# Kernel optimization log

Hardware: AMD Instinct MI355X
Metric: run time of the kernel (lower is better)

Reference implementation:

```python
import jax, jax.numpy as jnp
import numpy as np

K_CODES, D_DIM = 512, 64


def setup_inputs() -> dict:
    key = jax.random.key(0)
    k1, k2 = jax.random.split(key)
    x = jax.random.normal(k1, (32, D_DIM, 64, 64), dtype=jnp.float32)  # NCHW
    weight = jax.random.uniform(k2, (K_CODES, D_DIM), minval=-1.0 / K_CODES,
                                maxval=1.0 / K_CODES, dtype=jnp.float32)
    return {"x": x, "weight": weight}


def reference(x, weight):
    K = weight.shape[0]
    xp = jnp.transpose(x, (0, 2, 3, 1))          # [B, H, W, D]
    flat = xp.reshape(-1, weight.shape[1])       # [N, D]
    dist = (jnp.sum(flat * flat, axis=1, keepdims=True)
            + jnp.sum(weight * weight, axis=1)
            - 2.0 * flat @ weight.T)
    idx = jnp.argmin(dist, axis=1)               # [N]
    enc = jax.nn.one_hot(idx, K, dtype=jnp.float32)   # [N, K] one-hot scatter
    quantized = (enc @ weight).reshape(xp.shape)      # matmul codebook lookup
    commit_loss = jnp.mean(jnp.square(jax.lax.stop_gradient(quantized) - xp))
    vq_loss = jnp.mean(jnp.square(quantized - jax.lax.stop_gradient(xp)))
    loss = vq_loss + 1.0 * commit_loss           # commitment_cost = 1.0
    quant_st = xp + jax.lax.stop_gradient(quantized - xp)  # straight-through
    return (loss, jnp.transpose(quant_st, (0, 3, 1, 2)), enc, idx)
```

## Files before the change

kernel.cpp:

```cpp
#include <hip/hip_runtime.h>
#include <cfloat>

#define KC 512
#define DD 64
#define HW 4096
#define NPIX 131072
#define QSIZE 8388608
#define PXB 128
#define NBLK (NPIX / PXB)
#define NTH 512
#define MARGIN 4.0e-3f

typedef short short8 __attribute__((ext_vector_type(8)));
typedef float f32x4 __attribute__((ext_vector_type(4)));
typedef float nfloat4 __attribute__((ext_vector_type(4)));
typedef unsigned long long u64;

__device__ __forceinline__ unsigned short bf16_rne(float f) {
    unsigned int u = __float_as_uint(f);
    u += 0x7FFFu + ((u >> 16) & 1u);
    return (unsigned short)(u >> 16);
}

__global__ __launch_bounds__(NTH, 4) void vq_fused(
    const float* __restrict__ x, const float* __restrict__ w,
    float* __restrict__ out_q, float* __restrict__ out_enc,
    float* __restrict__ out_idx, double* __restrict__ partial) {

  __shared__ uint4 wlds[4096];
  __shared__ float w2s[KC];
  __shared__ u64 candm[PXB][8];
  __shared__ float Xs[PXB];
  __shared__ int sidx[PXB];
  __shared__ float sredf[8];

  const int tid = threadIdx.x;
  const int lane = tid & 63;
  const int wv = tid >> 6;
  const int bix = blockIdx.x;
  const int b = bix >> 5;
  const int p0 = (bix & 31) * PXB;
  const float* xt = x + (size_t)b * (DD * HW) + p0;

  {
    const int k = tid;
    const float* wk = w + k * DD;
    float r0 = __fmul_rn(wk[0], wk[0]), r1 = __fmul_rn(wk[1], wk[1]),
          r2 = __fmul_rn(wk[2], wk[2]), r3 = __fmul_rn(wk[3], wk[3]),
          r4 = __fmul_rn(wk[4], wk[4]), r5 = __fmul_rn(wk[5], wk[5]),
          r6 = __fmul_rn(wk[6], wk[6]), r7 = __fmul_rn(wk[7], wk[7]);
    #pragma unroll
    for (int i = 8; i < DD; i += 8) {
      r0 = __fadd_rn(r0, __fmul_rn(wk[i+0], wk[i+0]));
      r1 = __fadd_rn(r1, __fmul_rn(wk[i+1], wk[i+1]));
      r2 = __fadd_rn(r2, __fmul_rn(wk[i+2], wk[i+2]));
      r3 = __fadd_rn(r3, __fmul_rn(wk[i+3], wk[i+3]));
      r4 = __fadd_rn(r4, __fmul_rn(wk[i+4], wk[i+4]));
      r5 = __fadd_rn(r5, __fmul_rn(wk[i+5], wk[i+5]));
      r6 = __fadd_rn(r6, __fmul_rn(wk[i+6], wk[i+6]));
      r7 = __fadd_rn(r7, __fmul_rn(wk[i+7], wk[i+7]));
    }
    w2s[k] = __fadd_rn(__fadd_rn(__fadd_rn(r0, r1), __fadd_rn(r2, r3)),
                       __fadd_rn(__fadd_rn(r4, r5), __fadd_rn(r6, r7)));
  }

  for (int s = tid; s < 4096; s += NTH) {
    int ct = s >> 7, kc = (s >> 6) & 1, ln = s & 63;
    int n = ln & 15, q = ln >> 4;
    const float* wp = w + (ct * 16 + n) * DD + kc * 32 + q * 8;
    nfloat4 f0 = *(const nfloat4*)(wp);
    nfloat4 f1 = *(const nfloat4*)(wp + 4);
    uint4 u;
    u.x = (unsigned)bf16_rne(f0[0]) | ((unsigned)bf16_rne(f0[1]) << 16);
    u.y = (unsigned)bf16_rne(f0[2]) | ((unsigned)bf16_rne(f0[3]) << 16);
    u.z = (unsigned)bf16_rne(f1[0]) | ((unsigned)bf16_rne(f1[1]) << 16);
    u.w = (unsigned)bf16_rne(f1[2]) | ((unsigned)bf16_rne(f1[3]) << 16);
    wlds[s] = u;
  }
  for (int i = tid; i < PXB * 8; i += NTH) ((u64*)candm)[i] = 0;

  if (tid < PXB) {
    const float* xp = xt + tid;
    float r0 = __fmul_rn(xp[0*HW], xp[0*HW]), r1 = __fmul_rn(xp[1*HW], xp[1*HW]),
          r2 = __fmul_rn(xp[2*HW], xp[2*HW]), r3 = __fmul_rn(xp[3*HW], xp[3*HW]),
          r4 = __fmul_rn(xp[4*HW], xp[4*HW]), r5 = __fmul_rn(xp[5*HW], xp[5*HW]),
          r6 = __fmul_rn(xp[6*HW], xp[6*HW]), r7 = __fmul_rn(xp[7*HW], xp[7*HW]);
    #pragma unroll
    for (int i = 8; i < DD; i += 8) {
      r0 = __fadd_rn(r0, __fmul_rn(xp[(size_t)(i+0)*HW], xp[(size_t)(i+0)*HW]));
      r1 = __fadd_rn(r1, __fmul_rn(xp[(size_t)(i+1)*HW], xp[(size_t)(i+1)*HW]));
      r2 = __fadd_rn(r2, __fmul_rn(xp[(size_t)(i+2)*HW], xp[(size_t)(i+2)*HW]));
      r3 = __fadd_rn(r3, __fmul_rn(xp[(size_t)(i+3)*HW], xp[(size_t)(i+3)*HW]));
      r4 = __fadd_rn(r4, __fmul_rn(xp[(size_t)(i+4)*HW], xp[(size_t)(i+4)*HW]));
      r5 = __fadd_rn(r5, __fmul_rn(xp[(size_t)(i+5)*HW], xp[(size_t)(i+5)*HW]));
      r6 = __fadd_rn(r6, __fmul_rn(xp[(size_t)(i+6)*HW], xp[(size_t)(i+6)*HW]));
      r7 = __fadd_rn(r7, __fmul_rn(xp[(size_t)(i+7)*HW], xp[(size_t)(i+7)*HW]));
    }
    Xs[tid] = __fadd_rn(__fadd_rn(__fadd_rn(r0, r1), __fadd_rn(r2, r3)),
                        __fadd_rn(__fadd_rn(r4, r5), __fadd_rn(r6, r7)));
  }

  const int am = lane & 15, aq = lane >> 4;
  const float* xa = xt + wv * 16 + am;
  short8 a0, a1;
  #pragma unroll
  for (int j = 0; j < 8; ++j) {
    a0[j] = (short)bf16_rne(-2.0f * xa[(size_t)(aq * 8 + j) * HW]);
    a1[j] = (short)bf16_rne(-2.0f * xa[(size_t)(32 + aq * 8 + j) * HW]);
  }

  __syncthreads();

  const short8* wl8 = (const short8*)wlds;
  const int cn = lane & 15;

  float m0 = FLT_MAX, m1 = FLT_MAX, m2 = FLT_MAX, m3 = FLT_MAX;
  for (int ct = 0; ct < 32; ++ct) {
    float wk2 = w2s[ct * 16 + cn];
    f32x4 acc = {wk2, wk2, wk2, wk2};
    acc = __builtin_amdgcn_mfma_f32_16x16x32_bf16(a0, wl8[ct * 128 + lane], acc, 0, 0, 0);
    acc = __builtin_amdgcn_mfma_f32_16x16x32_bf16(a1, wl8[ct * 128 + 64 + lane], acc, 0, 0, 0);
    m0 = fminf(m0, acc[0]); m1 = fminf(m1, acc[1]);
    m2 = fminf(m2, acc[2]); m3 = fminf(m3, acc[3]);
  }
  #pragma unroll
  for (int s = 1; s < 16; s <<= 1) {
    m0 = fminf(m0, __shfl_xor(m0, s));
    m1 = fminf(m1, __shfl_xor(m1, s));
    m2 = fminf(m2, __shfl_xor(m2, s));
    m3 = fminf(m3, __shfl_xor(m3, s));
  }
  const float t0 = m0 + MARGIN, t1 = m1 + MARGIN,
              t2 = m2 + MARGIN, t3 = m3 + MARGIN;

  for (int ct = 0; ct < 32; ++ct) {
    float wk2 = w2s[ct * 16 + cn];
    f32x4 acc = {wk2, wk2, wk2, wk2};
    acc = __builtin_amdgcn_mfma_f32_16x16x32_bf16(a0, wl8[ct * 128 + lane], acc, 0, 0, 0);
    acc = __builtin_amdgcn_mfma_f32_16x16x32_bf16(a1, wl8[ct * 128 + 64 + lane], acc, 0, 0, 0);
    u64 bm0 = __ballot(acc[0] <= t0);
    u64 bm1 = __ballot(acc[1] <= t1);
    u64 bm2 = __ballot(acc[2] <= t2);
    u64 bm3 = __ballot(acc[3] <= t3);
    if (lane < 4) {
      u64 mk = (lane == 0) ? bm0 : (lane == 1) ? bm1 : (lane == 2) ? bm2 : bm3;
      int word = ct >> 2, sh = (ct & 3) * 16;
      #pragma unroll
      for (int q = 0; q < 4; ++q) {
        u64 bits = (mk >> (q * 16)) & 0xFFFFull;
        if (bits) candm[wv * 16 + q * 4 + lane][word] |= bits << sh;
      }
    }
  }
  __syncthreads();

  {
    const int px = tid >> 2, part = tid & 3;
    const float X = Xs[px];
    const float* xr = xt + px;
    float bestd = FLT_MAX; int bk = 1 << 30;
    for (int wd = part * 2; wd < part * 2 + 2; ++wd) {
      u64 msk = candm[px][wd];
      while (msk) {
        int bit = __ffsll((unsigned long long)msk) - 1;
        msk &= msk - 1;
        int k = wd * 64 + bit;
        const float* wp = w + k * DD;
        float P = 0.f;
        #pragma unroll
        for (int dc = 0; dc < 16; ++dc) {
          nfloat4 w4 = *(const nfloat4*)(wp + dc * 4);
          P = __fmaf_rn(xr[(size_t)(dc * 4 + 0) * HW], w4[0], P);
          P = __fmaf_rn(xr[(size_t)(dc * 4 + 1) * HW], w4[1], P);
          P = __fmaf_rn(xr[(size_t)(dc * 4 + 2) * HW], w4[2], P);
          P = __fmaf_rn(xr[(size_t)(dc * 4 + 3) * HW], w4[3], P);
        }
        float dist = __fsub_rn(__fadd_rn(X, w2s[k]), __fadd_rn(P, P));
        if (dist < bestd || (dist == bestd && k < bk)) { bestd = dist; bk = k; }
      }
    }
    float od = __shfl_down(bestd, 1); int ok = __shfl_down(bk, 1);
    if ((lane & 3) < 3 && (od < bestd || (od == bestd && ok < bk))) { bestd = od; bk = ok; }
    od = __shfl_down(bestd, 2); ok = __shfl_down(bk, 2);
    if ((lane & 3) < 2 && (od < bestd || (od == bestd && ok < bk))) { bestd = od; bk = ok; }
    if (part == 0) {
      sidx[px] = bk;
      out_idx[bix * PXB + px] = (float)bk;
    }
  }
  __syncthreads();

  float lsum = 0.f;
  float* qb = out_q + (size_t)b * (DD * HW) + p0;
  for (int i = tid; i < PXB * DD; i += NTH) {
    int d = i >> 7, pp = i & 127;
    float qv = w[sidx[pp] * DD + d];
    float dv = qv - xt[(size_t)d * HW + pp];
    lsum = __fmaf_rn(dv, dv, lsum);
    __builtin_nontemporal_store(qv, qb + (size_t)d * HW + pp);
  }
  #pragma unroll
  for (int off = 32; off > 0; off >>= 1) lsum += __shfl_down(lsum, off);
  if (lane == 0) sredf[wv] = lsum;
  __syncthreads();
  if (tid == 0) {
    double t = 0.0;
    #pragma unroll
    for (int i = 0; i < 8; ++i) t += (double)sredf[i];
    partial[bix] = t;
  }

  float* basep = out_enc + (size_t)bix * (PXB * KC);
  for (int t = tid; t < 16383; t += NTH) {
    int u = 3 + 4 * t;
    nfloat4 v;
    #pragma unroll
    for (int j = 0; j < 4; ++j) {
      int e = u + j;
      v[j] = (sidx[e >> 9] == (e & 511)) ? 1.0f : 0.0f;
    }
    __builtin_nontemporal_store(v, (nfloat4*)(basep + u));
  }
  if (tid < 3) basep[tid] = (sidx[0] == tid) ? 1.0f : 0.0f;
  else if (tid == 3) basep[PXB * KC - 1] = (sidx[127] == 511) ? 1.0f : 0.0f;
}

__global__ void finish_kernel(const double* __restrict__ partial,
                              float* __restrict__ out) {
  int t = threadIdx.x;
  double s = partial[t] + partial[t + 256] + partial[t + 512] + partial[t + 768];
  #pragma unroll
  for (int off = 32; off > 0; off >>= 1) s += __shfl_down(s, off);
  __shared__ double sr[4];
  if ((t & 63) == 0) sr[t >> 6] = s;
  __syncthreads();
  if (t == 0)
    out[0] = (float)(2.0 * (sr[0] + sr[1] + sr[2] + sr[3]) / (double)QSIZE);
}

extern "C" void kernel_launch(void* const* d_in, const int* in_sizes, int n_in,
                              void* d_out, int out_size, void* d_ws, size_t ws_size,
                              hipStream_t stream) {
  const float* x = (const float*)d_in[0];
  const float* w = (const float*)d_in[1];
  float* out = (float*)d_out;
  float* out_q = out + 1;
  float* out_enc = out_q + QSIZE;
  float* out_idx = out_enc + (size_t)NPIX * KC;

  double* partial = (double*)d_ws;

  vq_fused<<<NBLK, NTH, 0, stream>>>(x, w, out_q, out_enc, out_idx, partial);
  finish_kernel<<<1, 256, 0, stream>>>(partial, out);
}
```

Baseline: 391.3 us.

## Hoist codebook prep to a separate kernel and shrink blocks to raise occupancy

Codebook bf16 swizzling and squared-norm computation move out of the per-block prologue into a small prep kernel that writes to workspace. The main kernel drops its 64KB LDS copy of the codebook and reads MFMA B operands directly from global/L2, with 64-pixel blocks of 256 threads and a higher waves-per-EU hint. This removes redundant per-block conversion work and the LDS limit on occupancy. In exchange, every MFMA operand load now goes through the cache hierarchy instead of LDS, and there is an extra kernel launch.

```diff
diff --git a/kernel.cpp b/kernel.cpp
--- a/kernel.cpp
+++ b/kernel.cpp
@@ -6,9 +6,9 @@
 #define HW 4096
 #define NPIX 131072
 #define QSIZE 8388608
-#define PXB 128
+#define PXB 64
 #define NBLK (NPIX / PXB)
-#define NTH 512
+#define NTH 256
 #define MARGIN 4.0e-3f
 
 typedef short short8 __attribute__((ext_vector_type(8)));
@@ -22,29 +22,25 @@
     return (unsigned short)(u >> 16);
 }
 
-__global__ __launch_bounds__(NTH, 4) void vq_fused(
-    const float* __restrict__ x, const float* __restrict__ w,
-    float* __restrict__ out_q, float* __restrict__ out_enc,
-    float* __restrict__ out_idx, double* __restrict__ partial) {
-
-  __shared__ uint4 wlds[4096];
-  __shared__ float w2s[KC];
-  __shared__ u64 candm[PXB][8];
-  __shared__ float Xs[PXB];
-  __shared__ int sidx[PXB];
-  __shared__ float sredf[8];
-
-  const int tid = threadIdx.x;
-  const int lane = tid & 63;
-  const int wv = tid >> 6;
-  const int bix = blockIdx.x;
-  const int b = bix >> 5;
-  const int p0 = (bix & 31) * PXB;
-  const float* xt = x + (size_t)b * (DD * HW) + p0;
-
+__global__ __launch_bounds__(1024) void prep(
+    const float* __restrict__ w, float* __restrict__ w2g,
+    uint4* __restrict__ wswz) {
+  const int gt = blockIdx.x * 1024 + threadIdx.x;
   {
-    const int k = tid;
-    const float* wk = w + k * DD;
+    int ct = gt >> 7, kc = (gt >> 6) & 1, ln = gt & 63;
+    int n = ln & 15, q = ln >> 4;
+    const float* wp = w + (ct * 16 + n) * DD + kc * 32 + q * 8;
+    nfloat4 f0 = *(const nfloat4*)(wp);
+    nfloat4 f1 = *(const nfloat4*)(wp + 4);
+    uint4 u;
+    u.x = (unsigned)bf16_rne(f0[0]) | ((unsigned)bf16_rne(f0[1]) << 16);
+    u.y = (unsigned)bf16_rne(f0[2]) | ((unsigned)bf16_rne(f0[3]) << 16);
+    u.z = (unsigned)bf16_rne(f1[0]) | ((unsigned)bf16_rne(f1[1]) << 16);
+    u.w = (unsigned)bf16_rne(f1[2]) | ((unsigned)bf16_rne(f1[3]) << 16);
+    wswz[gt] = u;
+  }
+  if (gt < KC) {
+    const float* wk = w + gt * DD;
     float r0 = __fmul_rn(wk[0], wk[0]), r1 = __fmul_rn(wk[1], wk[1]),
           r2 = __fmul_rn(wk[2], wk[2]), r3 = __fmul_rn(wk[3], wk[3]),
           r4 = __fmul_rn(wk[4], wk[4]), r5 = __fmul_rn(wk[5], wk[5]),
@@ -60,24 +56,33 @@
       r6 = __fadd_rn(r6, __fmul_rn(wk[i+6], wk[i+6]));
       r7 = __fadd_rn(r7, __fmul_rn(wk[i+7], wk[i+7]));
     }
-    w2s[k] = __fadd_rn(__fadd_rn(__fadd_rn(r0, r1), __fadd_rn(r2, r3)),
-                       __fadd_rn(__fadd_rn(r4, r5), __fadd_rn(r6, r7)));
-  }
-
-  for (int s = tid; s < 4096; s += NTH) {
-    int ct = s >> 7, kc = (s >> 6) & 1, ln = s & 63;
-    int n = ln & 15, q = ln >> 4;
-    const float* wp = w + (ct * 16 + n) * DD + kc * 32 + q * 8;
-    nfloat4 f0 = *(const nfloat4*)(wp);
-    nfloat4 f1 = *(const nfloat4*)(wp + 4);
-    uint4 u;
-    u.x = (unsigned)bf16_rne(f0[0]) | ((unsigned)bf16_rne(f0[1]) << 16);
-    u.y = (unsigned)bf16_rne(f0[2]) | ((unsigned)bf16_rne(f0[3]) << 16);
-    u.z = (unsigned)bf16_rne(f1[0]) | ((unsigned)bf16_rne(f1[1]) << 16);
-    u.w = (unsigned)bf16_rne(f1[2]) | ((unsigned)bf16_rne(f1[3]) << 16);
-    wlds[s] = u;
-  }
+    w2g[gt] = __fadd_rn(__fadd_rn(__fadd_rn(r0, r1), __fadd_rn(r2, r3)),
+                        __fadd_rn(__fadd_rn(r4, r5), __fadd_rn(r6, r7)));
+  }
+}
+
+__global__ __launch_bounds__(NTH, 6) void vq_fused(
+    const float* __restrict__ x, const float* __restrict__ w,
+    const float* __restrict__ w2g, const uint4* __restrict__ wswz,
+    float* __restrict__ out_q, float* __restrict__ out_enc,
+    float* __restrict__ out_idx, double* __restrict__ partial) {
+
+  __shared__ u64 candm[PXB][8];
+  __shared__ float w2l[KC];
+  __shared__ float Xs[PXB];
+  __shared__ int sidx[PXB];
+  __shared__ float sredf[4];
+
+  const int tid = threadIdx.x;
+  const int lane = tid & 63;
+  const int wv = tid >> 6;
+  const int bix = blockIdx.x;
+  const int b = bix >> 6;
+  const int p0 = (bix & 63) * PXB;
+  const float* xt = x + (size_t)b * (DD * HW) + p0;
+
   for (int i = tid; i < PXB * 8; i += NTH) ((u64*)candm)[i] = 0;
+  w2l[tid] = w2g[tid]; w2l[tid + 256] = w2g[tid + 256];
 
   if (tid < PXB) {
     const float* xp = xt + tid;
@@ -111,15 +116,15 @@
 
   __syncthreads();
 
-  const short8* wl8 = (const short8*)wlds;
+  const short8* gw8 = (const short8*)wswz;
   const int cn = lane & 15;
 
   float m0 = FLT_MAX, m1 = FLT_MAX, m2 = FLT_MAX, m3 = FLT_MAX;
   for (int ct = 0; ct < 32; ++ct) {
-    float wk2 = w2s[ct * 16 + cn];
+    float wk2 = w2l[ct * 16 + cn];
     f32x4 acc = {wk2, wk2, wk2, wk2};
-    acc = __builtin_amdgcn_mfma_f32_16x16x32_bf16(a0, wl8[ct * 128 + lane], acc, 0, 0, 0);
-    acc = __builtin_amdgcn_mfma_f32_16x16x32_bf16(a1, wl8[ct * 128 + 64 + lane], acc, 0, 0, 0);
+    acc = __builtin_amdgcn_mfma_f32_16x16x32_bf16(a0, gw8[ct * 128 + lane], acc, 0, 0, 0);
+    acc = __builtin_amdgcn_mfma_f32_16x16x32_bf16(a1, gw8[ct * 128 + 64 + lane], acc, 0, 0, 0);
     m0 = fminf(m0, acc[0]); m1 = fminf(m1, acc[1]);
     m2 = fminf(m2, acc[2]); m3 = fminf(m3, acc[3]);
   }
@@ -134,10 +139,10 @@
               t2 = m2 + MARGIN, t3 = m3 + MARGIN;
 
   for (int ct = 0; ct < 32; ++ct) {
-    float wk2 = w2s[ct * 16 + cn];
+    float wk2 = w2l[ct * 16 + cn];
     f32x4 acc = {wk2, wk2, wk2, wk2};
-    acc = __builtin_amdgcn_mfma_f32_16x16x32_bf16(a0, wl8[ct * 128 + lane], acc, 0, 0, 0);
-    acc = __builtin_amdgcn_mfma_f32_16x16x32_bf16(a1, wl8[ct * 128 + 64 + lane], acc, 0, 0, 0);
+    acc = __builtin_amdgcn_mfma_f32_16x16x32_bf16(a0, gw8[ct * 128 + lane], acc, 0, 0, 0);
+    acc = __builtin_amdgcn_mfma_f32_16x16x32_bf16(a1, gw8[ct * 128 + 64 + lane], acc, 0, 0, 0);
     u64 bm0 = __ballot(acc[0] <= t0);
     u64 bm1 = __ballot(acc[1] <= t1);
     u64 bm2 = __ballot(acc[2] <= t2);
@@ -175,7 +180,7 @@
           P = __fmaf_rn(xr[(size_t)(dc * 4 + 2) * HW], w4[2], P);
           P = __fmaf_rn(xr[(size_t)(dc * 4 + 3) * HW], w4[3], P);
         }
-        float dist = __fsub_rn(__fadd_rn(X, w2s[k]), __fadd_rn(P, P));
+        float dist = __fsub_rn(__fadd_rn(X, w2l[k]), __fadd_rn(P, P));
         if (dist < bestd || (dist == bestd && k < bk)) { bestd = dist; bk = k; }
       }
     }
@@ -193,7 +198,7 @@
   float lsum = 0.f;
   float* qb = out_q + (size_t)b * (DD * HW) + p0;
   for (int i = tid; i < PXB * DD; i += NTH) {
-    int d = i >> 7, pp = i & 127;
+    int d = i >> 6, pp = i & 63;
     float qv = w[sidx[pp] * DD + d];
     float dv = qv - xt[(size_t)d * HW + pp];
     lsum = __fmaf_rn(dv, dv, lsum);
@@ -203,15 +208,12 @@
   for (int off = 32; off > 0; off >>= 1) lsum += __shfl_down(lsum, off);
   if (lane == 0) sredf[wv] = lsum;
   __syncthreads();
-  if (tid == 0) {
-    double t = 0.0;
-    #pragma unroll
-    for (int i = 0; i < 8; ++i) t += (double)sredf[i];
-    partial[bix] = t;
-  }
+  if (tid == 0)
+    partial[bix] = (double)sredf[0] + (double)sredf[1]
+                 + (double)sredf[2] + (double)sredf[3];
 
   float* basep = out_enc + (size_t)bix * (PXB * KC);
-  for (int t = tid; t < 16383; t += NTH) {
+  for (int t = tid; t < 8191; t += NTH) {
     int u = 3 + 4 * t;
     nfloat4 v;
     #pragma unroll
@@ -222,13 +224,15 @@
     __builtin_nontemporal_store(v, (nfloat4*)(basep + u));
   }
   if (tid < 3) basep[tid] = (sidx[0] == tid) ? 1.0f : 0.0f;
-  else if (tid == 3) basep[PXB * KC - 1] = (sidx[127] == 511) ? 1.0f : 0.0f;
+  else if (tid == 3) basep[PXB * KC - 1] = (sidx[PXB - 1] == 511) ? 1.0f : 0.0f;
 }
 
 __global__ void finish_kernel(const double* __restrict__ partial,
                               float* __restrict__ out) {
   int t = threadIdx.x;
-  double s = partial[t] + partial[t + 256] + partial[t + 512] + partial[t + 768];
+  double s = 0.0;
+  #pragma unroll
+  for (int i = 0; i < 8; ++i) s += partial[t + 256 * i];
   #pragma unroll
   for (int off = 32; off > 0; off >>= 1) s += __shfl_down(s, off);
   __shared__ double sr[4];
@@ -249,7 +253,10 @@
   float* out_idx = out_enc + (size_t)NPIX * KC;
 
   double* partial = (double*)d_ws;
-
-  vq_fused<<<NBLK, NTH, 0, stream>>>(x, w, out_q, out_enc, out_idx, partial);
+  float* w2g = (float*)((char*)d_ws + 16384);
+  uint4* wswz = (uint4*)((char*)d_ws + 18432);
+
+  prep<<<4, 1024, 0, stream>>>(w, w2g, wswz);
+  vq_fused<<<NBLK, NTH, 0, stream>>>(x, w, w2g, wswz, out_q, out_enc, out_idx, partial);
   finish_kernel<<<1, 256, 0, stream>>>(partial, out);
 }
```

Result: slower. 429.9 us (+9.9%).
